# Optimization experiments

Measured on AMD Instinct MI355X. Metric: run time of the kernel, lower is better.

The kernel has to match this reference:

```python
import jax, jax.numpy as jnp
import numpy as np

B, MAXLEN, H, T, NC = 2048, 1000, 512, 21, 10  # T = 21 one-hot classes -> seq_len


def _uniform(key, shape, bound):
    return jax.random.uniform(key, shape, jnp.float32, -bound, bound)


def setup_inputs() -> dict:
    key = jax.random.key(0)
    ks = jax.random.split(key, 16)
    k = 1.0 / np.sqrt(H)
    inp = {
        "x": jax.random.randint(ks[0], (B, MAXLEN), 0, 21),
        # layer 0: input size MAXLEN; stacked over 2 directions
        "w_ih0": _uniform(ks[1], (2, 4 * H, MAXLEN), k),
        "w_hh0": _uniform(ks[2], (2, 4 * H, H), k),
        "b_ih0": _uniform(ks[3], (2, 4 * H), k),
        "b_hh0": _uniform(ks[4], (2, 4 * H), k),
        # layer 1: input size 2H
        "w_ih1": _uniform(ks[5], (2, 4 * H, 2 * H), k),
        "w_hh1": _uniform(ks[6], (2, 4 * H, H), k),
        "b_ih1": _uniform(ks[7], (2, 4 * H), k),
        "b_hh1": _uniform(ks[8], (2, 4 * H), k),
        # emb: Linear(21 -> 1) over the seq axis
        "emb_w": _uniform(ks[9], (1, T), 1.0 / np.sqrt(T)),
        "emb_b": _uniform(ks[10], (1,), 1.0 / np.sqrt(T)),
        # fc: Linear(2H -> NC)
        "fc_w": _uniform(ks[11], (NC, 2 * H), 1.0 / np.sqrt(2 * H)),
        "fc_b": _uniform(ks[12], (NC,), 1.0 / np.sqrt(2 * H)),
    }
    return inp


def _lstm_dir(xs, w_ih, w_hh, b_ih, b_hh, reverse):
    # xs: [T, B, I]; PyTorch gate order i, f, g, o
    gx = jnp.einsum('tbi,gi->tbg', xs, w_ih) + b_ih + b_hh  # [T,B,4H]
    h_dim = w_hh.shape[1]
    bsz = xs.shape[1]

    def step(carry, g_t):
        h, c = carry
        g = g_t + h @ w_hh.T
        i, f, gg, o = jnp.split(g, 4, axis=-1)
        c = jax.nn.sigmoid(f) * c + jax.nn.sigmoid(i) * jnp.tanh(gg)
        h = jax.nn.sigmoid(o) * jnp.tanh(c)
        return (h, c), h

    init = (jnp.zeros((bsz, h_dim), xs.dtype), jnp.zeros((bsz, h_dim), xs.dtype))
    _, hs = jax.lax.scan(step, init, gx, reverse=reverse)
    return hs  # [T,B,H], time-aligned (matches torch bidirectional output)


def _bilstm_layer(xs, w_ih, w_hh, b_ih, b_hh):
    hf = _lstm_dir(xs, w_ih[0], w_hh[0], b_ih[0], b_hh[0], reverse=False)
    hb = _lstm_dir(xs, w_ih[1], w_hh[1], b_ih[1], b_hh[1], reverse=True)
    return jnp.concatenate([hf, hb], axis=-1)  # [T,B,2H]


def reference(x, w_ih0, w_hh0, b_ih0, b_hh0, w_ih1, w_hh1, b_ih1, b_hh1,
              emb_w, emb_b, fc_w, fc_b):
    xoh = jax.nn.one_hot(x, 21, dtype=jnp.float32)       # [B, MAXLEN, 21]
    seq = xoh.transpose(2, 0, 1)                          # [T=21, B, MAXLEN]
    seq = _bilstm_layer(seq, w_ih0, w_hh0, b_ih0, b_hh0)  # [T,B,2H]
    seq = _bilstm_layer(seq, w_ih1, w_hh1, b_ih1, b_hh1)  # [T,B,2H]
    # emb: Linear(21->1) applied along seq axis, then squeeze -> [B, 2H]
    z = jnp.einsum('tbh,t->bh', seq, emb_w[0]) + emb_b[0]
    return z @ fc_w.T + fc_b                              # [B, NC]
```

## Files before the change

kernel.cpp:

```cpp
#include <hip/hip_runtime.h>
#include <hip/hip_bf16.h>
#include <cstdint>
#include <cstddef>

#define B_SZ    2048
#define H_SZ    512
#define G4      2048
#define TSTEPS  21
#define MAXLEN  1000
#define KIN     1024
#define NCLS    10

#define BM    128
#define BN    128
#define BKS   32
#define LDSKS 40
#define NITS  16
#define NITG  32
#define GP2   68
#define STEPBUF (3 * BM * LDSKS)
#define GXBUF   (2 * BM * LDSKS)
#define SMEM_BYTES 61440

typedef short bf16x8 __attribute__((ext_vector_type(8)));
typedef float f32x4  __attribute__((ext_vector_type(4)));
typedef unsigned short ushort8 __attribute__((ext_vector_type(8)));

__device__ __forceinline__ unsigned short f2bf(float f) {
  __hip_bfloat16 h = __float2bfloat16(f);
  unsigned short u; __builtin_memcpy(&u, &h, sizeof(u)); return u;
}
__device__ __forceinline__ float bf2f(unsigned short u) {
  __hip_bfloat16 h; __builtin_memcpy(&h, &u, sizeof(h)); return __bfloat162float(h);
}
__device__ __forceinline__ float sigmoidf_(float x) {
  x = fminf(fmaxf(x, -30.f), 30.f);
  return 1.f / (1.f + __expf(-x));
}
__device__ __forceinline__ float tanhf_(float x) {
  float xc = fminf(fmaxf(x, -15.f), 15.f);
  float e = __expf(2.f * xc);
  return (e - 1.f) / (e + 1.f);
}
__device__ __forceinline__ void bar_lgkm() {
  asm volatile("s_waitcnt lgkmcnt(0)" ::: "memory");
  __builtin_amdgcn_s_barrier();
  __builtin_amdgcn_sched_barrier(0);
}
__device__ __forceinline__ int rbase_of(int p) { return (p & 3) * H_SZ + (p >> 2); }

__global__ void prep_rec_kernel(const float* __restrict__ w_hh,
                                unsigned short* __restrict__ Bhi,
                                unsigned short* __restrict__ Blo) {
  size_t idx = (size_t)blockIdx.x * blockDim.x + threadIdx.x;
  const size_t total = (size_t)2 * G4 * H_SZ;
  if (idx >= total) return;
  int k  = (int)(idx % H_SZ);
  size_t rowidx = idx / H_SZ;
  int p  = (int)(rowidx % G4);
  int dd = (int)(rowidx / G4);
  float w = w_hh[((size_t)dd * G4 + rbase_of(p)) * H_SZ + k];
  unsigned short h = f2bf(w);
  Bhi[idx] = h;
  Blo[idx] = f2bf(w - bf2f(h));
}

__global__ void prep_in0_kernel(const float* __restrict__ w_ih0,
                                unsigned short* __restrict__ Bin0) {
  size_t idx = (size_t)blockIdx.x * blockDim.x + threadIdx.x;
  const size_t total = (size_t)2 * G4 * KIN;
  if (idx >= total) return;
  int k  = (int)(idx % KIN);
  size_t rowidx = idx / KIN;
  int p  = (int)(rowidx % G4);
  int dd = (int)(rowidx / G4);
  float v = (k < MAXLEN) ? w_ih0[((size_t)dd * G4 + rbase_of(p)) * MAXLEN + k] : 0.f;
  Bin0[idx] = f2bf(v);
}

__global__ void prep_in1_kernel(const float* __restrict__ w_ih1,
                                unsigned short* __restrict__ Bin1) {
  size_t idx = (size_t)blockIdx.x * blockDim.x + threadIdx.x;
  const size_t total = (size_t)2 * G4 * KIN;
  if (idx >= total) return;
  int k  = (int)(idx % KIN);
  size_t rowidx = idx / KIN;
  int p  = (int)(rowidx % G4);
  int dd = (int)(rowidx / G4);
  Bin1[idx] = f2bf(w_ih1[((size_t)dd * G4 + rbase_of(p)) * KIN + k]);
}

__global__ void prep_b_kernel(const float* __restrict__ b_ih0,
                              const float* __restrict__ b_hh0,
                              const float* __restrict__ b_ih1,
                              const float* __restrict__ b_hh1,
                              float* __restrict__ bias0,
                              float* __restrict__ bias1) {
  int idx = blockIdx.x * blockDim.x + threadIdx.x;
  if (idx >= 2 * G4) return;
  int p  = idx % G4;
  int dd = idx / G4;
  int src = dd * G4 + rbase_of(p);
  bias0[idx] = b_ih0[src] + b_hh0[src];
  bias1[idx] = b_ih1[src] + b_hh1[src];
}

__global__ void prep_x_kernel(const int* __restrict__ x,
                              unsigned int* __restrict__ bits) {
  int idx = blockIdx.x * blockDim.x + threadIdx.x;
  if (idx >= B_SZ * 32) return;
  int b = idx >> 5;
  int w = idx & 31;
  const int* xr = x + (size_t)b * MAXLEN + w * 32;
  int xv[32];
#pragma unroll
  for (int j = 0; j < 32; ++j) {
    int k = w * 32 + j;
    xv[j] = (k < MAXLEN) ? xr[j] : -1;
  }
#pragma unroll
  for (int t = 0; t < TSTEPS; ++t) {
    unsigned int m = 0;
#pragma unroll
    for (int j = 0; j < 32; ++j)
      m |= (xv[j] == t) ? (1u << j) : 0u;
    bits[((size_t)t * B_SZ + b) * 32 + w] = m;
  }
}

template <int LAYER>
__global__ __launch_bounds__(512, 4)
void fused_kernel(const unsigned int* __restrict__ xbits,
                  const unsigned short* __restrict__ seq_in,
                  const unsigned short* __restrict__ Bin,
                  const unsigned short* __restrict__ Bhrec,
                  const unsigned short* __restrict__ Blrec,
                  const float* __restrict__ bias,
                  const unsigned short* __restrict__ h_in,
                  unsigned short* __restrict__ h_out,
                  float* __restrict__ c_st,
                  unsigned short* __restrict__ seq_out,
                  float* __restrict__ zacc,
                  const float* __restrict__ emb_w,
                  int step) {
  extern __shared__ char smraw[];
  unsigned short* buf0s = (unsigned short*)smraw;
  unsigned short* buf1s = buf0s + STEPBUF;
  unsigned short* buf0g = (unsigned short*)smraw;
  unsigned short* buf1g = buf0g + GXBUF;
  float*          gc    = (float*)smraw;

  const int tid  = threadIdx.x;
  const int lane = tid & 63;
  const int wave = tid >> 6;
  const int wr   = wave >> 2;
  const int wc   = wave & 3;
  const int q    = lane >> 4;
  const int r16  = lane & 15;

  const int sid  = blockIdx.x;
  const int xcd  = sid & 7;
  const int slot = sid >> 3;
  const int nb   = xcd * 2 + (slot & 1);
  const int mb   = (slot >> 1) & 15;
  const int d    = slot >> 5;
  const int tcur = d ? (TSTEPS - 1 - step) : step;
  const int n0   = nb * BN;
  const int m0   = mb * BM;

  const unsigned short* Bh_mat = Bhrec + (size_t)d * G4 * H_SZ;
  const unsigned short* Bl_mat = Blrec + (size_t)d * G4 * H_SZ;
  const unsigned short* Ah     = h_in + (size_t)d * B_SZ * H_SZ;
  const unsigned short* Bmat   = Bin + (size_t)d * G4 * KIN;
  const unsigned char*  xrow   = (const unsigned char*)xbits + ((size_t)tcur * B_SZ) * (KIN / 8);
  const unsigned short* Asrc   = seq_in + (size_t)tcur * B_SZ * (2 * H_SZ);

  float bval[2];
#pragma unroll
  for (int nt = 0; nt < 2; ++nt)
    bval[nt] = bias[d * G4 + n0 + wc * 32 + nt * 16 + r16];

  f32x4 acc[4][2];
#pragma unroll
  for (int mt = 0; mt < 4; ++mt)
#pragma unroll
    for (int nt = 0; nt < 2; ++nt) {
      f32x4 z = {0.f, 0.f, 0.f, 0.f};
      acc[mt][nt] = z;
    }

  const int rstg = tid >> 2;
  const int ostg = (tid & 3) * 8;

  ushort8 pbA, paA, pbB, paB;
  unsigned int bvA, bvB;
  auto gloadA = [&](int kt) {
    const int k0 = kt * BKS;
    pbA = *(const ushort8*)(Bmat + (size_t)(n0 + rstg) * KIN + k0 + ostg);
    if (LAYER == 0) {
      bvA = xrow[(size_t)(m0 + rstg) * (KIN / 8) + (k0 + ostg) / 8];
    } else {
      paA = *(const ushort8*)(Asrc + (size_t)(m0 + rstg) * (2 * H_SZ) + k0 + ostg);
    }
  };
  auto gloadB = [&](int kt) {
    const int k0 = kt * BKS;
    pbB = *(const ushort8*)(Bmat + (size_t)(n0 + rstg) * KIN + k0 + ostg);
    if (LAYER == 0) {
      bvB = xrow[(size_t)(m0 + rstg) * (KIN / 8) + (k0 + ostg) / 8];
    } else {
      paB = *(const ushort8*)(Asrc + (size_t)(m0 + rstg) * (2 * H_SZ) + k0 + ostg);
    }
  };
  auto expand = [&](unsigned int bv, unsigned short* dst) {
    unsigned int pk[4];
#pragma unroll
    for (int e = 0; e < 4; ++e) {
      pk[e] = (((bv >> (2 * e)) & 1u) ? 0x3F80u : 0u)
            | (((bv >> (2 * e + 1)) & 1u) ? 0x3F800000u : 0u);
    }
    *(uint4*)dst = make_uint4(pk[0], pk[1], pk[2], pk[3]);
  };
  auto gstoreA = [&](unsigned short* sA) {
    unsigned short* sB = sA + BM * LDSKS;
    if (LAYER == 0) expand(bvA, sA + rstg * LDSKS + ostg);
    else            *(ushort8*)(sA + rstg * LDSKS + ostg) = paA;
    *(ushort8*)(sB + rstg * LDSKS + ostg) = pbA;
  };
  auto gstoreB = [&](unsigned short* sA) {
    unsigned short* sB = sA + BM * LDSKS;
    if (LAYER == 0) expand(bvB, sA + rstg * LDSKS + ostg);
    else            *(ushort8*)(sA + rstg * LDSKS + ostg) = paB;
    *(ushort8*)(sB + rstg * LDSKS + ostg) = pbB;
  };
  auto gcompute = [&](const unsigned short* sA) {
    const unsigned short* sB = sA + BM * LDSKS;
    bf16x8 af[4], bh[2];
#pragma unroll
    for (int mt = 0; mt < 4; ++mt)
      af[mt] = *(const bf16x8*)(sA + (wr * 64 + mt * 16 + r16) * LDSKS + q * 8);
#pragma unroll
    for (int nt = 0; nt < 2; ++nt)
      bh[nt] = *(const bf16x8*)(sB + (wc * 32 + nt * 16 + r16) * LDSKS + q * 8);
#pragma unroll
    for (int mt = 0; mt < 4; ++mt)
#pragma unroll
      for (int nt = 0; nt < 2; ++nt)
        acc[mt][nt] = __builtin_amdgcn_mfma_f32_16x16x32_bf16(af[mt], bh[nt], acc[mt][nt], 0, 0, 0);
  };

  ushort8 pbhA, pblA, pvaA, pbhB, pblB, pvaB;
  auto sloadA = [&](int kt) {
    const int k0 = kt * BKS;
    pbhA = *(const ushort8*)(Bh_mat + (size_t)(n0 + rstg) * H_SZ + k0 + ostg);
    pblA = *(const ushort8*)(Bl_mat + (size_t)(n0 + rstg) * H_SZ + k0 + ostg);
    pvaA = *(const ushort8*)(Ah + (size_t)(m0 + rstg) * H_SZ + k0 + ostg);
  };
  auto sloadB = [&](int kt) {
    const int k0 = kt * BKS;
    pbhB = *(const ushort8*)(Bh_mat + (size_t)(n0 + rstg) * H_SZ + k0 + ostg);
    pblB = *(const ushort8*)(Bl_mat + (size_t)(n0 + rstg) * H_SZ + k0 + ostg);
    pvaB = *(const ushort8*)(Ah + (size_t)(m0 + rstg) * H_SZ + k0 + ostg);
  };
  auto sstoreA = [&](unsigned short* sA) {
    *(ushort8*)(sA + rstg * LDSKS + ostg)                  = pvaA;
    *(ushort8*)(sA + BM * LDSKS + rstg * LDSKS + ostg)     = pbhA;
    *(ushort8*)(sA + 2 * BM * LDSKS + rstg * LDSKS + ostg) = pblA;
  };
  auto sstoreB = [&](unsigned short* sA) {
    *(ushort8*)(sA + rstg * LDSKS + ostg)                  = pvaB;
    *(ushort8*)(sA + BM * LDSKS + rstg * LDSKS + ostg)     = pbhB;
    *(ushort8*)(sA + 2 * BM * LDSKS + rstg * LDSKS + ostg) = pblB;
  };
  auto scompute = [&](const unsigned short* sA) {
    const unsigned short* sBh = sA + BM * LDSKS;
    const unsigned short* sBl = sBh + BM * LDSKS;
    bf16x8 af[4], bh[2];
#pragma unroll
    for (int mt = 0; mt < 4; ++mt)
      af[mt] = *(const bf16x8*)(sA + (wr * 64 + mt * 16 + r16) * LDSKS + q * 8);
#pragma unroll
    for (int nt = 0; nt < 2; ++nt)
      bh[nt] = *(const bf16x8*)(sBh + (wc * 32 + nt * 16 + r16) * LDSKS + q * 8);
#pragma unroll
    for (int mt = 0; mt < 4; ++mt)
#pragma unroll
      for (int nt = 0; nt < 2; ++nt)
        acc[mt][nt] = __builtin_amdgcn_mfma_f32_16x16x32_bf16(af[mt], bh[nt], acc[mt][nt], 0, 0, 0);
    bf16x8 bl[2];
#pragma unroll
    for (int nt = 0; nt < 2; ++nt)
      bl[nt] = *(const bf16x8*)(sBl + (wc * 32 + nt * 16 + r16) * LDSKS + q * 8);
#pragma unroll
    for (int mt = 0; mt < 4; ++mt)
#pragma unroll
      for (int nt = 0; nt < 2; ++nt)
        acc[mt][nt] = __builtin_amdgcn_mfma_f32_16x16x32_bf16(af[mt], bl[nt], acc[mt][nt], 0, 0, 0);
  };

  float cpre[2][4];
  float zpre[2][4];

  gloadA(0);
  gloadB(1);
  for (int kt2 = 0; kt2 < NITG; kt2 += 2) {
    gstoreA(buf0g);
    bar_lgkm();
    if (kt2 + 2 < NITG) gloadA(kt2 + 2); else sloadA(0);
    gcompute(buf0g);

    gstoreB(buf1g);
    bar_lgkm();
    if (kt2 + 3 < NITG) gloadB(kt2 + 3); else sloadB(1);
    gcompute(buf1g);
  }
  bar_lgkm();

  for (int kt2 = 0; kt2 < NITS; kt2 += 2) {
    sstoreA(buf0s);
    bar_lgkm();
    if (kt2 + 2 < NITS) sloadA(kt2 + 2);
    scompute(buf0s);

    sstoreB(buf1s);
    bar_lgkm();
    if (kt2 + 3 < NITS) sloadB(kt2 + 3);
    if (kt2 == NITS - 6) {
      const int jb = nb * 32;
#pragma unroll
      for (int cc = 0; cc < 2; ++cc)
#pragma unroll
        for (int it = 0; it < 4; ++it) {
          int cell = it * 512 + tid;
          int rl = cell >> 4, jq = cell & 15;
          int b = m0 + rl;
          int j = jb + cc * 16 + jq;
          cpre[cc][it] = c_st[((size_t)d * B_SZ + b) * H_SZ + j];
          if (LAYER == 1)
            zpre[cc][it] = zacc[(size_t)b * (2 * H_SZ) + d * H_SZ + j];
        }
    }
    scompute(buf1s);
  }
  __syncthreads();

  const int jbase = nb * 32;
  const float ew = (LAYER == 1) ? emb_w[tcur] : 0.f;

#pragma unroll
  for (int cc = 0; cc < 2; ++cc) {
    if ((wc >> 1) == cc) {
#pragma unroll
      for (int mt = 0; mt < 4; ++mt)
#pragma unroll
        for (int nt = 0; nt < 2; ++nt)
#pragma unroll
          for (int r = 0; r < 4; ++r) {
            int ml = wr * 64 + mt * 16 + q * 4 + r;
            int nl = (wc & 1) * 32 + nt * 16 + r16;
            gc[ml * GP2 + nl] = acc[mt][nt][r] + bval[nt];
          }
    }
    __syncthreads();

#pragma unroll
    for (int it = 0; it < 4; ++it) {
      int cell = it * 512 + tid;
      int rl = cell >> 4, jq = cell & 15;
      int b = m0 + rl;
      int j = jbase + cc * 16 + jq;
      float4 g = *(const float4*)(&gc[rl * GP2 + jq * 4]);
      float si = sigmoidf_(g.x);
      float sf = sigmoidf_(g.y);
      float tg = tanhf_(g.z);
      float so = sigmoidf_(g.w);
      size_t cidx = ((size_t)d * B_SZ + b) * H_SZ + j;
      float cn = sf * cpre[cc][it] + si * tg;
      float hv = so * tanhf_(cn);
      c_st[cidx] = cn;
      h_out[cidx] = f2bf(hv);
      if (LAYER == 0) {
        seq_out[((size_t)tcur * B_SZ + b) * (2 * H_SZ) + d * H_SZ + j] = f2bf(hv);
      } else {
        zacc[(size_t)b * (2 * H_SZ) + d * H_SZ + j] = zpre[cc][it] + ew * hv;
      }
    }
    if (cc == 0) __syncthreads();
  }
}

__global__ __launch_bounds__(256)
void final_kernel(const float* __restrict__ zacc,
                  const float* __restrict__ emb_b,
                  const float* __restrict__ fc_w,
                  const float* __restrict__ fc_b,
                  float* __restrict__ out) {
  const int b = blockIdx.x;
  const int tid = threadIdx.x;
  const int c0 = tid * 4;

  const float zb = emb_b[0];
  const float4 z4 = *(const float4*)(zacc + (size_t)b * (2 * H_SZ) + c0);
  float z0 = z4.x + zb, z1 = z4.y + zb, z2 = z4.z + zb, z3 = z4.w + zb;

  float part[NCLS];
#pragma unroll
  for (int nc = 0; nc < NCLS; ++nc) {
    const float4 f = *(const float4*)(fc_w + (size_t)nc * (2 * H_SZ) + c0);
    part[nc] = z0 * f.x + z1 * f.y + z2 * f.z + z3 * f.w;
  }
#pragma unroll
  for (int nc = 0; nc < NCLS; ++nc)
#pragma unroll
    for (int off2 = 32; off2 > 0; off2 >>= 1)
      part[nc] += __shfl_down(part[nc], off2);

  __shared__ float red[4][NCLS];
  if ((tid & 63) == 0) {
#pragma unroll
    for (int nc = 0; nc < NCLS; ++nc) red[tid >> 6][nc] = part[nc];
  }
  __syncthreads();
  if (tid < NCLS) {
    float s = red[0][tid] + red[1][tid] + red[2][tid] + red[3][tid] + fc_b[tid];
    out[b * NCLS + tid] = s;
  }
}

extern "C" void kernel_launch(void* const* d_in, const int* in_sizes, int n_in,
                              void* d_out, int out_size, void* d_ws, size_t ws_size,
                              hipStream_t stream) {
  (void)in_sizes; (void)n_in; (void)out_size; (void)ws_size;

  const int*   x     = (const int*)d_in[0];
  const float* w_ih0 = (const float*)d_in[1];
  const float* w_hh0 = (const float*)d_in[2];
  const float* b_ih0 = (const float*)d_in[3];
  const float* b_hh0 = (const float*)d_in[4];
  const float* w_ih1 = (const float*)d_in[5];
  const float* w_hh1 = (const float*)d_in[6];
  const float* b_ih1 = (const float*)d_in[7];
  const float* b_hh1 = (const float*)d_in[8];
  const float* emb_w = (const float*)d_in[9];
  const float* emb_b = (const float*)d_in[10];
  const float* fc_w  = (const float*)d_in[11];
  const float* fc_b  = (const float*)d_in[12];

  char* ws = (char*)d_ws;
  size_t off = 0;
  auto alloc = [&](size_t bytes) -> void* {
    void* p = ws + off;
    off += (bytes + 255) & ~(size_t)255;
    return p;
  };
  const size_t bin_b  = (size_t)2 * G4 * KIN * 2;
  const size_t brec_b = (size_t)2 * G4 * H_SZ * 2;
  const size_t xb_b   = (size_t)TSTEPS * B_SZ * 32 * 4;
  const size_t h_b    = (size_t)2 * B_SZ * H_SZ * 2;
  const size_t c_b    = (size_t)2 * B_SZ * H_SZ * 4;
  const size_t seq_b  = (size_t)TSTEPS * B_SZ * (2 * H_SZ) * 2;
  const size_t z_b    = (size_t)B_SZ * (2 * H_SZ) * 4;

  unsigned short* Bin0  = (unsigned short*)alloc(bin_b);
  unsigned short* Bin1  = (unsigned short*)alloc(bin_b);
  unsigned short* Bh0   = (unsigned short*)alloc(brec_b);
  unsigned short* Bl0   = (unsigned short*)alloc(brec_b);
  unsigned short* Bh1   = (unsigned short*)alloc(brec_b);
  unsigned short* Bl1   = (unsigned short*)alloc(brec_b);
  float*          bias0 = (float*)alloc((size_t)2 * G4 * 4);
  float*          bias1 = (float*)alloc((size_t)2 * G4 * 4);
  unsigned int*   xbits = (unsigned int*)alloc(xb_b);
  unsigned short* hA    = (unsigned short*)alloc(h_b);
  unsigned short* hB    = (unsigned short*)alloc(h_b);
  float*          cst   = (float*)alloc(c_b);
  unsigned short* seq0  = (unsigned short*)alloc(seq_b);
  float*          zacc  = (float*)Bin0;

  {
    size_t ti = (size_t)2 * G4 * KIN;
    prep_in0_kernel<<<(int)((ti + 255) / 256), 256, 0, stream>>>(w_ih0, Bin0);
    prep_in1_kernel<<<(int)((ti + 255) / 256), 256, 0, stream>>>(w_ih1, Bin1);
    size_t tr = (size_t)2 * G4 * H_SZ;
    prep_rec_kernel<<<(int)((tr + 255) / 256), 256, 0, stream>>>(w_hh0, Bh0, Bl0);
    prep_rec_kernel<<<(int)((tr + 255) / 256), 256, 0, stream>>>(w_hh1, Bh1, Bl1);
    prep_b_kernel<<<16, 256, 0, stream>>>(b_ih0, b_hh0, b_ih1, b_hh1, bias0, bias1);
    prep_x_kernel<<<(B_SZ * 32 + 255) / 256, 256, 0, stream>>>(x, xbits);
  }

  hipMemsetAsync(hA, 0, h_b, stream);
  hipMemsetAsync(cst, 0, c_b, stream);
  for (int s = 0; s < TSTEPS; ++s) {
    const unsigned short* hin  = (s & 1) ? hB : hA;
    unsigned short*       hout = (s & 1) ? hA : hB;
    fused_kernel<0><<<512, 512, SMEM_BYTES, stream>>>(
        xbits, nullptr, Bin0, Bh0, Bl0, bias0, hin, hout, cst,
        seq0, nullptr, nullptr, s);
  }

  hipMemsetAsync(hA, 0, h_b, stream);
  hipMemsetAsync(cst, 0, c_b, stream);
  hipMemsetAsync(zacc, 0, z_b, stream);
  for (int s = 0; s < TSTEPS; ++s) {
    const unsigned short* hin  = (s & 1) ? hB : hA;
    unsigned short*       hout = (s & 1) ? hA : hB;
    fused_kernel<1><<<512, 512, SMEM_BYTES, stream>>>(
        nullptr, seq0, Bin1, Bh1, Bl1, bias1, hin, hout, cst,
        nullptr, zacc, emb_w, s);
  }

  final_kernel<<<B_SZ, 256, 0, stream>>>(zacc, emb_b, fc_w, fc_b, (float*)d_out);
}
```

Before: 2.176 ms.

## Load A operand fragments directly from global into registers, bypassing LDS

The A-side operands (one-hot expanded input, layer-1 sequence, and recurrent h) are now loaded by each wave straight from global memory into MFMA fragment registers instead of being staged through shared memory. This halves and shrinks LDS buffers (61440 to 40960 bytes) and removes LDS stores and reads for A. The next-tile prefetch is also moved after the compute call. In exchange, A rows are loaded redundantly by each of the 4 column waves, global loads are narrower and less coalesced, and register pressure rises.

After: 7.284 ms. 3.35x slower.

```diff
diff --git a/kernel.cpp b/kernel.cpp
--- a/kernel.cpp
+++ b/kernel.cpp
@@ -18,9 +18,9 @@
 #define NITS  16
 #define NITG  32
 #define GP2   68
-#define STEPBUF (3 * BM * LDSKS)
-#define GXBUF   (2 * BM * LDSKS)
-#define SMEM_BYTES 61440
+#define STEPB (2 * BM * LDSKS)
+#define GXB   (BM * LDSKS)
+#define SMEM_BYTES 40960
 
 typedef short bf16x8 __attribute__((ext_vector_type(8)));
 typedef float f32x4  __attribute__((ext_vector_type(4)));
@@ -46,6 +46,14 @@
   asm volatile("s_waitcnt lgkmcnt(0)" ::: "memory");
   __builtin_amdgcn_s_barrier();
   __builtin_amdgcn_sched_barrier(0);
+}
+__device__ __forceinline__ bf16x8 expand_oh(unsigned int bv) {
+  union { unsigned int u[4]; bf16x8 v; } r;
+#pragma unroll
+  for (int e = 0; e < 4; ++e)
+    r.u[e] = (((bv >> (2 * e)) & 1u) ? 0x3F80u : 0u)
+           | (((bv >> (2 * e + 1)) & 1u) ? 0x3F800000u : 0u);
+  return r.v;
 }
 __device__ __forceinline__ int rbase_of(int p) { return (p & 3) * H_SZ + (p >> 2); }
 
@@ -144,10 +152,10 @@
                   const float* __restrict__ emb_w,
                   int step) {
   extern __shared__ char smraw[];
-  unsigned short* buf0s = (unsigned short*)smraw;
-  unsigned short* buf1s = buf0s + STEPBUF;
-  unsigned short* buf0g = (unsigned short*)smraw;
-  unsigned short* buf1g = buf0g + GXBUF;
+  unsigned short* bufg0 = (unsigned short*)smraw;
+  unsigned short* bufg1 = bufg0 + GXB;
+  unsigned short* bufs0 = (unsigned short*)smraw;
+  unsigned short* bufs1 = bufs0 + STEPB;
   float*          gc    = (float*)smraw;
 
   const int tid  = threadIdx.x;
@@ -175,6 +183,12 @@
   const unsigned char*  xrow   = (const unsigned char*)xbits + ((size_t)tcur * B_SZ) * (KIN / 8);
   const unsigned short* Asrc   = seq_in + (size_t)tcur * B_SZ * (2 * H_SZ);
 
+  const unsigned short* ah_base = Ah + (size_t)(m0 + wr * 64 + r16) * H_SZ + q * 8;
+  const unsigned short* as_base = (LAYER == 1)
+      ? (Asrc + (size_t)(m0 + wr * 64 + r16) * (2 * H_SZ) + q * 8) : (const unsigned short*)nullptr;
+  const unsigned char*  xb_base = (LAYER == 0)
+      ? (xrow + (size_t)(m0 + wr * 64 + r16) * (KIN / 8) + q) : (const unsigned char*)nullptr;
+
   float bval[2];
 #pragma unroll
   for (int nt = 0; nt < 2; ++nt)
@@ -192,53 +206,45 @@
   const int rstg = tid >> 2;
   const int ostg = (tid & 3) * 8;
 
-  ushort8 pbA, paA, pbB, paB;
-  unsigned int bvA, bvB;
+  ushort8 pbA, pbB;
+  bf16x8 gaA[4], gaB[4];
+  unsigned int gbA[4], gbB[4];
   auto gloadA = [&](int kt) {
-    const int k0 = kt * BKS;
-    pbA = *(const ushort8*)(Bmat + (size_t)(n0 + rstg) * KIN + k0 + ostg);
+    pbA = *(const ushort8*)(Bmat + (size_t)(n0 + rstg) * KIN + kt * BKS + ostg);
     if (LAYER == 0) {
-      bvA = xrow[(size_t)(m0 + rstg) * (KIN / 8) + (k0 + ostg) / 8];
+#pragma unroll
+      for (int mt = 0; mt < 4; ++mt)
+        gbA[mt] = xb_base[(size_t)mt * 16 * (KIN / 8) + kt * 4];
     } else {
-      paA = *(const ushort8*)(Asrc + (size_t)(m0 + rstg) * (2 * H_SZ) + k0 + ostg);
+#pragma unroll
+      for (int mt = 0; mt < 4; ++mt)
+        gaA[mt] = *(const bf16x8*)(as_base + (size_t)mt * 16 * (2 * H_SZ) + kt * BKS);
     }
   };
   auto gloadB = [&](int kt) {
-    const int k0 = kt * BKS;
-    pbB = *(const ushort8*)(Bmat + (size_t)(n0 + rstg) * KIN + k0 + ostg);
+    pbB = *(const ushort8*)(Bmat + (size_t)(n0 + rstg) * KIN + kt * BKS + ostg);
     if (LAYER == 0) {
-      bvB = xrow[(size_t)(m0 + rstg) * (KIN / 8) + (k0 + ostg) / 8];
+#pragma unroll
+      for (int mt = 0; mt < 4; ++mt)
+        gbB[mt] = xb_base[(size_t)mt * 16 * (KIN / 8) + kt * 4];
     } else {
-      paB = *(const ushort8*)(Asrc + (size_t)(m0 + rstg) * (2 * H_SZ) + k0 + ostg);
-    }
-  };
-  auto expand = [&](unsigned int bv, unsigned short* dst) {
-    unsigned int pk[4];
-#pragma unroll
-    for (int e = 0; e < 4; ++e) {
-      pk[e] = (((bv >> (2 * e)) & 1u) ? 0x3F80u : 0u)
-            | (((bv >> (2 * e + 1)) & 1u) ? 0x3F800000u : 0u);
-    }
-    *(uint4*)dst = make_uint4(pk[0], pk[1], pk[2], pk[3]);
-  };
-  auto gstoreA = [&](unsigned short* sA) {
-    unsigned short* sB = sA + BM * LDSKS;
-    if (LAYER == 0) expand(bvA, sA + rstg * LDSKS + ostg);
-    else            *(ushort8*)(sA + rstg * LDSKS + ostg) = paA;
-    *(ushort8*)(sB + rstg * LDSKS + ostg) = pbA;
-  };
-  auto gstoreB = [&](unsigned short* sA) {
-    unsigned short* sB = sA + BM * LDSKS;
-    if (LAYER == 0) expand(bvB, sA + rstg * LDSKS + ostg);
-    else            *(ushort8*)(sA + rstg * LDSKS + ostg) = paB;
-    *(ushort8*)(sB + rstg * LDSKS + ostg) = pbB;
-  };
-  auto gcompute = [&](const unsigned short* sA) {
-    const unsigned short* sB = sA + BM * LDSKS;
-    bf16x8 af[4], bh[2];
-#pragma unroll
-    for (int mt = 0; mt < 4; ++mt)
-      af[mt] = *(const bf16x8*)(sA + (wr * 64 + mt * 16 + r16) * LDSKS + q * 8);
+#pragma unroll
+      for (int mt = 0; mt < 4; ++mt)
+        gaB[mt] = *(const bf16x8*)(as_base + (size_t)mt * 16 * (2 * H_SZ) + kt * BKS);
+    }
+  };
+  auto gstoreA = [&](unsigned short* sB) { *(ushort8*)(sB + rstg * LDSKS + ostg) = pbA; };
+  auto gstoreB = [&](unsigned short* sB) { *(ushort8*)(sB + rstg * LDSKS + ostg) = pbB; };
+  auto gcomputeA = [&](const unsigned short* sB) {
+    bf16x8 af[4];
+    if (LAYER == 0) {
+#pragma unroll
+      for (int mt = 0; mt < 4; ++mt) af[mt] = expand_oh(gbA[mt]);
+    } else {
+#pragma unroll
+      for (int mt = 0; mt < 4; ++mt) af[mt] = gaA[mt];
+    }
+    bf16x8 bh[2];
 #pragma unroll
     for (int nt = 0; nt < 2; ++nt)
       bh[nt] = *(const bf16x8*)(sB + (wc * 32 + nt * 16 + r16) * LDSKS + q * 8);
@@ -248,37 +254,54 @@
       for (int nt = 0; nt < 2; ++nt)
         acc[mt][nt] = __builtin_amdgcn_mfma_f32_16x16x32_bf16(af[mt], bh[nt], acc[mt][nt], 0, 0, 0);
   };
-
-  ushort8 pbhA, pblA, pvaA, pbhB, pblB, pvaB;
+  auto gcomputeB = [&](const unsigned short* sB) {
+    bf16x8 af[4];
+    if (LAYER == 0) {
+#pragma unroll
+      for (int mt = 0; mt < 4; ++mt) af[mt] = expand_oh(gbB[mt]);
+    } else {
+#pragma unroll
+      for (int mt = 0; mt < 4; ++mt) af[mt] = gaB[mt];
+    }
+    bf16x8 bh[2];
+#pragma unroll
+    for (int nt = 0; nt < 2; ++nt)
+      bh[nt] = *(const bf16x8*)(sB + (wc * 32 + nt * 16 + r16) * LDSKS + q * 8);
+#pragma unroll
+    for (int mt = 0; mt < 4; ++mt)
+#pragma unroll
+      for (int nt = 0; nt < 2; ++nt)
+        acc[mt][nt] = __builtin_amdgcn_mfma_f32_16x16x32_bf16(af[mt], bh[nt], acc[mt][nt], 0, 0, 0);
+  };
+
+  ushort8 pbhA, pblA, pbhB, pblB;
+  bf16x8 saA[4], saB[4];
   auto sloadA = [&](int kt) {
-    const int k0 = kt * BKS;
-    pbhA = *(const ushort8*)(Bh_mat + (size_t)(n0 + rstg) * H_SZ + k0 + ostg);
-    pblA = *(const ushort8*)(Bl_mat + (size_t)(n0 + rstg) * H_SZ + k0 + ostg);
-    pvaA = *(const ushort8*)(Ah + (size_t)(m0 + rstg) * H_SZ + k0 + ostg);
+    pbhA = *(const ushort8*)(Bh_mat + (size_t)(n0 + rstg) * H_SZ + kt * BKS + ostg);
+    pblA = *(const ushort8*)(Bl_mat + (size_t)(n0 + rstg) * H_SZ + kt * BKS + ostg);
+#pragma unroll
+    for (int mt = 0; mt < 4; ++mt)
+      saA[mt] = *(const bf16x8*)(ah_base + (size_t)mt * 16 * H_SZ + kt * BKS);
   };
   auto sloadB = [&](int kt) {
-    const int k0 = kt * BKS;
-    pbhB = *(const ushort8*)(Bh_mat + (size_t)(n0 + rstg) * H_SZ + k0 + ostg);
-    pblB = *(const ushort8*)(Bl_mat + (size_t)(n0 + rstg) * H_SZ + k0 + ostg);
-    pvaB = *(const ushort8*)(Ah + (size_t)(m0 + rstg) * H_SZ + k0 + ostg);
-  };
-  auto sstoreA = [&](unsigned short* sA) {
-    *(ushort8*)(sA + rstg * LDSKS + ostg)                  = pvaA;
-    *(ushort8*)(sA + BM * LDSKS + rstg * LDSKS + ostg)     = pbhA;
-    *(ushort8*)(sA + 2 * BM * LDSKS + rstg * LDSKS + ostg) = pblA;
-  };
-  auto sstoreB = [&](unsigned short* sA) {
-    *(ushort8*)(sA + rstg * LDSKS + ostg)                  = pvaB;
-    *(ushort8*)(sA + BM * LDSKS + rstg * LDSKS + ostg)     = pbhB;
-    *(ushort8*)(sA + 2 * BM * LDSKS + rstg * LDSKS + ostg) = pblB;
-  };
-  auto scompute = [&](const unsigned short* sA) {
-    const unsigned short* sBh = sA + BM * LDSKS;
-    const unsigned short* sBl = sBh + BM * LDSKS;
-    bf16x8 af[4], bh[2];
-#pragma unroll
-    for (int mt = 0; mt < 4; ++mt)
-      af[mt] = *(const bf16x8*)(sA + (wr * 64 + mt * 16 + r16) * LDSKS + q * 8);
+    pbhB = *(const ushort8*)(Bh_mat + (size_t)(n0 + rstg) * H_SZ + kt * BKS + ostg);
+    pblB = *(const ushort8*)(Bl_mat + (size_t)(n0 + rstg) * H_SZ + kt * BKS + ostg);
+#pragma unroll
+    for (int mt = 0; mt < 4; ++mt)
+      saB[mt] = *(const bf16x8*)(ah_base + (size_t)mt * 16 * H_SZ + kt * BKS);
+  };
+  auto sstoreA = [&](unsigned short* sBuf) {
+    *(ushort8*)(sBuf + rstg * LDSKS + ostg)              = pbhA;
+    *(ushort8*)(sBuf + BM * LDSKS + rstg * LDSKS + ostg) = pblA;
+  };
+  auto sstoreB = [&](unsigned short* sBuf) {
+    *(ushort8*)(sBuf + rstg * LDSKS + ostg)              = pbhB;
+    *(ushort8*)(sBuf + BM * LDSKS + rstg * LDSKS + ostg) = pblB;
+  };
+  auto scomputeA = [&](const unsigned short* sBuf) {
+    const unsigned short* sBh = sBuf;
+    const unsigned short* sBl = sBuf + BM * LDSKS;
+    bf16x8 bh[2];
 #pragma unroll
     for (int nt = 0; nt < 2; ++nt)
       bh[nt] = *(const bf16x8*)(sBh + (wc * 32 + nt * 16 + r16) * LDSKS + q * 8);
@@ -286,7 +309,7 @@
     for (int mt = 0; mt < 4; ++mt)
 #pragma unroll
       for (int nt = 0; nt < 2; ++nt)
-        acc[mt][nt] = __builtin_amdgcn_mfma_f32_16x16x32_bf16(af[mt], bh[nt], acc[mt][nt], 0, 0, 0);
+        acc[mt][nt] = __builtin_amdgcn_mfma_f32_16x16x32_bf16(saA[mt], bh[nt], acc[mt][nt], 0, 0, 0);
     bf16x8 bl[2];
 #pragma unroll
     for (int nt = 0; nt < 2; ++nt)
@@ -295,7 +318,29 @@
     for (int mt = 0; mt < 4; ++mt)
 #pragma unroll
       for (int nt = 0; nt < 2; ++nt)
-        acc[mt][nt] = __builtin_amdgcn_mfma_f32_16x16x32_bf16(af[mt], bl[nt], acc[mt][nt], 0, 0, 0);
+        acc[mt][nt] = __builtin_amdgcn_mfma_f32_16x16x32_bf16(saA[mt], bl[nt], acc[mt][nt], 0, 0, 0);
+  };
+  auto scomputeB = [&](const unsigned short* sBuf) {
+    const unsigned short* sBh = sBuf;
+    const unsigned short* sBl = sBuf + BM * LDSKS;
+    bf16x8 bh[2];
+#pragma unroll
+    for (int nt = 0; nt < 2; ++nt)
+      bh[nt] = *(const bf16x8*)(sBh + (wc * 32 + nt * 16 + r16) * LDSKS + q * 8);
+#pragma unroll
+    for (int mt = 0; mt < 4; ++mt)
+#pragma unroll
+      for (int nt = 0; nt < 2; ++nt)
+        acc[mt][nt] = __builtin_amdgcn_mfma_f32_16x16x32_bf16(saB[mt], bh[nt], acc[mt][nt], 0, 0, 0);
+    bf16x8 bl[2];
+#pragma unroll
+    for (int nt = 0; nt < 2; ++nt)
+      bl[nt] = *(const bf16x8*)(sBl + (wc * 32 + nt * 16 + r16) * LDSKS + q * 8);
+#pragma unroll
+    for (int mt = 0; mt < 4; ++mt)
+#pragma unroll
+      for (int nt = 0; nt < 2; ++nt)
+        acc[mt][nt] = __builtin_amdgcn_mfma_f32_16x16x32_bf16(saB[mt], bl[nt], acc[mt][nt], 0, 0, 0);
   };
 
   float cpre[2][4];
@@ -304,27 +349,28 @@
   gloadA(0);
   gloadB(1);
   for (int kt2 = 0; kt2 < NITG; kt2 += 2) {
-    gstoreA(buf0g);
+    gstoreA(bufg0);
     bar_lgkm();
-    if (kt2 + 2 < NITG) gloadA(kt2 + 2); else sloadA(0);
-    gcompute(buf0g);
-
-    gstoreB(buf1g);
+    gcomputeA(bufg0);
+    if (kt2 + 2 < NITG) gloadA(kt2 + 2);
+    else                sloadA(0);
+
+    gstoreB(bufg1);
     bar_lgkm();
-    if (kt2 + 3 < NITG) gloadB(kt2 + 3); else sloadB(1);
-    gcompute(buf1g);
+    gcomputeB(bufg1);
+    if (kt2 + 3 < NITG) gloadB(kt2 + 3);
+    else                sloadB(1);
   }
   bar_lgkm();
 
   for (int kt2 = 0; kt2 < NITS; kt2 += 2) {
-    sstoreA(buf0s);
+    sstoreA(bufs0);
     bar_lgkm();
+    scomputeA(bufs0);
     if (kt2 + 2 < NITS) sloadA(kt2 + 2);
-    scompute(buf0s);
-
-    sstoreB(buf1s);
+
+    sstoreB(bufs1);
     bar_lgkm();
-    if (kt2 + 3 < NITS) sloadB(kt2 + 3);
     if (kt2 == NITS - 6) {
       const int jb = nb * 32;
 #pragma unroll
@@ -340,7 +386,8 @@
             zpre[cc][it] = zacc[(size_t)b * (2 * H_SZ) + d * H_SZ + j];
         }
     }
-    scompute(buf1s);
+    scomputeB(bufs1);
+    if (kt2 + 3 < NITS) sloadB(kt2 + 3);
   }
   __syncthreads();
 
```
